# Kernel tuning notes

Hardware: AMD Instinct MI355X
Metric: run time of the kernel (lower is better)

## Reference

```python
import jax, jax.numpy as jnp
import numpy as np

N, D, HF, HS, E, TOPK = 4096, 1024, 2048, 4096, 8, 2
NUM_FRACTAL = 4  # int(8 * 0.5)
EPS_RMS = 1e-6


def setup_inputs() -> dict:
    key = jax.random.key(0)
    ks = jax.random.split(key, 9)
    s = 0.02
    return {
        "x": jax.random.normal(ks[0], (N, D), dtype=jnp.float32),
        "router_w": jax.random.normal(ks[1], (E, D), dtype=jnp.float32) * s,
        "frac_rms": jnp.ones((NUM_FRACTAL, D), jnp.float32),
        "frac_w1": jax.random.normal(ks[2], (NUM_FRACTAL, HF, D), dtype=jnp.float32) * s,
        "frac_w2": jax.random.normal(ks[3], (NUM_FRACTAL, D, HF), dtype=jnp.float32) * s,
        "frac_w3": jax.random.normal(ks[4], (NUM_FRACTAL, HF, D), dtype=jnp.float32) * s,
        "frac_gamma": jnp.full((NUM_FRACTAL, D), 1e-5, jnp.float32),
        "sw_w1": jax.random.normal(ks[5], (E - NUM_FRACTAL, HS, D), dtype=jnp.float32) * s,
        "sw_w2": jax.random.normal(ks[6], (E - NUM_FRACTAL, D, HS), dtype=jnp.float32) * s,
        "sw_w3": jax.random.normal(ks[7], (E - NUM_FRACTAL, HS, D), dtype=jnp.float32) * s,
    }


def _rmsnorm(x, w):
    return x * jax.lax.rsqrt(jnp.mean(x * x, axis=-1, keepdims=True) + EPS_RMS) * w


def _swiglu(x, w1, w2, w3):
    # torch Linear: y = x @ W.T
    return (jax.nn.silu(x @ w1.T) * (x @ w3.T)) @ w2.T


def _fractal(x, rms_w, w1, w2, w3, gamma):
    # depth=1 FractalBlock, eval mode (stochastic depth = identity)
    xn = _rmsnorm(x, rms_w)
    xn = xn + _swiglu(xn, w1, w2, w3)
    return gamma * xn + x


def _moe(x, router_w, frac_rms, frac_w1, frac_w2, frac_w3, frac_gamma,
         sw_w1, sw_w2, sw_w3):
    gate_logits = x @ router_w.T                      # [N, E]
    weights = jax.nn.softmax(gate_logits, axis=-1)
    top_w, top_i = jax.lax.top_k(weights, TOPK)        # [N, K]
    top_w = top_w / jnp.maximum(jnp.sum(top_w, axis=-1, keepdims=True), 1e-9)
    # dense combine weights: zero for unrouted experts (mathematically equal
    # to the gather/index_add dispatch in the original)
    combine = jnp.zeros((x.shape[0], E), x.dtype).at[
        jnp.arange(x.shape[0])[:, None], top_i].add(top_w)  # [N, E]

    out = jnp.zeros_like(x)
    for e in range(NUM_FRACTAL):
        out = out + combine[:, e:e + 1] * _fractal(
            x, frac_rms[e], frac_w1[e], frac_w2[e], frac_w3[e], frac_gamma[e])
    for j in range(E - NUM_FRACTAL):
        e = NUM_FRACTAL + j
        out = out + combine[:, e:e + 1] * _swiglu(x, sw_w1[j], sw_w2[j], sw_w3[j])
    return out


def reference(x, router_w, frac_rms, frac_w1, frac_w2, frac_w3, frac_gamma,
              sw_w1, sw_w2, sw_w3):
    return _moe(x, router_w, frac_rms, frac_w1, frac_w2, frac_w3, frac_gamma,
                sw_w1, sw_w2, sw_w3)
```

## Files before the change

kernel.cpp:

```cpp
#include <hip/hip_runtime.h>
#include <stdint.h>

#define N_TOK 4096
#define DIM   1024
#define HFRAC 2048
#define HSW   4096
#define NEXP  8
#define NFRAC 4
#define TOPK  2
#define TOTAL_ROWS (N_TOK * TOPK)
#define PAD_ROWS   (TOTAL_ROWS + 128)

typedef unsigned short u16;
typedef __bf16 bf16x8 __attribute__((ext_vector_type(8)));
typedef float  floatx4 __attribute__((ext_vector_type(4)));

struct alignas(8)  us4 { u16 v[4]; };
struct alignas(16) us8 { u16 v[8]; };

__device__ __forceinline__ u16 f32_to_bf16_raw(float f) {
    union { float f; uint32_t u; } v; v.f = f;
    uint32_t u = v.u;
    uint32_t r = 0x7FFFu + ((u >> 16) & 1u);
    return (u16)((u + r) >> 16);
}
__device__ __forceinline__ float bf16_raw_to_f32(u16 h) {
    union { uint32_t u; float f; } v; v.u = ((uint32_t)h) << 16;
    return v.f;
}

__device__ __forceinline__ int sw_addr(int row, int chunk) {
    return row * 64 + ((chunk ^ (row & 7)) << 3);
}

__global__ __launch_bounds__(256) void router_kernel(
    const float* __restrict__ x, const float* __restrict__ rw,
    int* __restrict__ re, float* __restrict__ rc, int* __restrict__ counts) {
    const int token = blockIdx.x * 4 + (threadIdx.x >> 6);
    const int lane  = threadIdx.x & 63;
    const float* xr = x + (size_t)token * DIM;

    float acc[NEXP];
#pragma unroll
    for (int e = 0; e < NEXP; ++e) acc[e] = 0.0f;
#pragma unroll
    for (int i = 0; i < DIM / 64; ++i) {
        int k = lane + i * 64;
        float xv = xr[k];
#pragma unroll
        for (int e = 0; e < NEXP; ++e) acc[e] += xv * rw[e * DIM + k];
    }
#pragma unroll
    for (int e = 0; e < NEXP; ++e) {
#pragma unroll
        for (int off = 32; off > 0; off >>= 1) acc[e] += __shfl_down(acc[e], off);
    }
    if (lane == 0) {
        float mx = acc[0];
#pragma unroll
        for (int e = 1; e < NEXP; ++e) mx = fmaxf(mx, acc[e]);
        float w[NEXP]; float s = 0.0f;
#pragma unroll
        for (int e = 0; e < NEXP; ++e) { w[e] = expf(acc[e] - mx); s += w[e]; }
        float inv = 1.0f / s;
#pragma unroll
        for (int e = 0; e < NEXP; ++e) w[e] *= inv;
        int i1 = 0;
#pragma unroll
        for (int e = 1; e < NEXP; ++e) if (w[e] > w[i1]) i1 = e;
        int i2 = (i1 == 0) ? 1 : 0;
#pragma unroll
        for (int e = 0; e < NEXP; ++e) if (e != i1 && w[e] > w[i2]) i2 = e;
        float denom = fmaxf(w[i1] + w[i2], 1e-9f);
        re[token]         = i1; rc[token]         = w[i1] / denom;
        re[N_TOK + token] = i2; rc[N_TOK + token] = w[i2] / denom;
        atomicAdd(&counts[i1], 1);
        atomicAdd(&counts[i2], 1);
    }
}

__global__ void offsets_kernel(const int* __restrict__ counts,
                               int* __restrict__ offs) {
    if (threadIdx.x == 0 && blockIdx.x == 0) {
        int a = 0;
#pragma unroll
        for (int e = 0; e < NEXP; ++e) { offs[e] = a; a += counts[e]; }
    }
}

__global__ __launch_bounds__(256) void scatter_kernel(
    const int* __restrict__ re, const float* __restrict__ rc,
    const int* __restrict__ offs, int* __restrict__ cursor,
    int* __restrict__ rowtok, float* __restrict__ co) {
    int token = blockIdx.x * 256 + threadIdx.x;
#pragma unroll
    for (int slot = 0; slot < TOPK; ++slot) {
        int e = re[slot * N_TOK + token];
        int i = atomicAdd(&cursor[e], 1);
        int r = offs[e] + i;
        rowtok[r] = token | (slot << 16);
        co[r]     = rc[slot * N_TOK + token];
    }
}

__global__ __launch_bounds__(256) void gather_norm_kernel(
    const float* __restrict__ x, const float* __restrict__ frac_rms,
    const int* __restrict__ rowtok, const int* __restrict__ offs,
    u16* __restrict__ Ag) {
    const int r   = blockIdx.x;
    const int tid = threadIdx.x;
    if (r >= TOTAL_ROWS) {
        us4 z = {0, 0, 0, 0};
        reinterpret_cast<us4*>(Ag + (size_t)r * DIM)[tid] = z;
        return;
    }
    int e = 0;
#pragma unroll
    for (int i = 1; i < NEXP; ++i) if (r >= offs[i]) e = i;
    const int token = rowtok[r] & 0xFFFF;
    float4 v = reinterpret_cast<const float4*>(x + (size_t)token * DIM)[tid];
    if (e < NFRAC) {
        float ss = v.x * v.x + v.y * v.y + v.z * v.z + v.w * v.w;
#pragma unroll
        for (int off = 32; off > 0; off >>= 1) ss += __shfl_down(ss, off);
        __shared__ float red[4];
        if ((tid & 63) == 0) red[tid >> 6] = ss;
        __syncthreads();
        float scale = rsqrtf((red[0] + red[1] + red[2] + red[3]) * (1.0f / DIM) + 1e-6f);
        float4 wv = reinterpret_cast<const float4*>(frac_rms + (size_t)e * DIM)[tid];
        v.x *= scale * wv.x; v.y *= scale * wv.y;
        v.z *= scale * wv.z; v.w *= scale * wv.w;
    }
    us4 o = { f32_to_bf16_raw(v.x), f32_to_bf16_raw(v.y),
              f32_to_bf16_raw(v.z), f32_to_bf16_raw(v.w) };
    reinterpret_cast<us4*>(Ag + (size_t)r * DIM)[tid] = o;
}

#define BM 128
#define BN 64
#define BK 64

__global__ __launch_bounds__(256) void gemm1_kernel(
    const u16* __restrict__ Ag,
    const float* __restrict__ frac_w1, const float* __restrict__ frac_w3,
    const float* __restrict__ sw_w1,   const float* __restrict__ sw_w3,
    u16* __restrict__ gbuf,
    const int* __restrict__ counts, const int* __restrict__ offs) {
    const int e   = blockIdx.z;
    const int cnt = counts[e];
    const int m0  = blockIdx.y * BM;
    if (m0 >= cnt) return;
    const int Ne = (e < NFRAC) ? HFRAC : HSW;
    const int n0 = blockIdx.x * BN;
    if (n0 >= Ne) return;
    const int rowbase = offs[e];
    const float* W1 = (e < NFRAC) ? frac_w1 + (size_t)e * HFRAC * DIM
                                  : sw_w1 + (size_t)(e - NFRAC) * HSW * DIM;
    const float* W3 = (e < NFRAC) ? frac_w3 + (size_t)e * HFRAC * DIM
                                  : sw_w3 + (size_t)(e - NFRAC) * HSW * DIM;
    const u16* A = Ag + (size_t)(rowbase + m0) * DIM;

    __shared__ u16 sA[BM * BK];
    __shared__ u16 sB1[BN * BK];
    __shared__ u16 sB3[BN * BK];

    const int tid  = threadIdx.x;
    const int wave = tid >> 6;
    const int lane = tid & 63;

    floatx4 acc1[2][4], acc3[2][4];
    floatx4 zero = { 0.f, 0.f, 0.f, 0.f };
#pragma unroll
    for (int mt = 0; mt < 2; ++mt)
#pragma unroll
        for (int nt = 0; nt < 4; ++nt) { acc1[mt][nt] = zero; acc3[mt][nt] = zero; }

    for (int k0 = 0; k0 < DIM; k0 += BK) {
#pragma unroll
        for (int it = 0; it < 4; ++it) {
            int idx = it * 2048 + tid * 8;
            int r = idx >> 6, c = idx & 63;
            int4 v = *reinterpret_cast<const int4*>(A + (size_t)r * DIM + k0 + c);
            *reinterpret_cast<int4*>(&sA[sw_addr(r, c >> 3)]) = v;
        }
#pragma unroll
        for (int it = 0; it < 2; ++it) {
            int idx = it * 2048 + tid * 8;
            int r = idx >> 6, c = idx & 63;
            size_t go = (size_t)(n0 + r) * DIM + k0 + c;
            float4 a1 = *reinterpret_cast<const float4*>(W1 + go);
            float4 b1 = *reinterpret_cast<const float4*>(W1 + go + 4);
            float4 a3 = *reinterpret_cast<const float4*>(W3 + go);
            float4 b3 = *reinterpret_cast<const float4*>(W3 + go + 4);
            us8 o1 = { f32_to_bf16_raw(a1.x), f32_to_bf16_raw(a1.y),
                       f32_to_bf16_raw(a1.z), f32_to_bf16_raw(a1.w),
                       f32_to_bf16_raw(b1.x), f32_to_bf16_raw(b1.y),
                       f32_to_bf16_raw(b1.z), f32_to_bf16_raw(b1.w) };
            us8 o3 = { f32_to_bf16_raw(a3.x), f32_to_bf16_raw(a3.y),
                       f32_to_bf16_raw(a3.z), f32_to_bf16_raw(a3.w),
                       f32_to_bf16_raw(b3.x), f32_to_bf16_raw(b3.y),
                       f32_to_bf16_raw(b3.z), f32_to_bf16_raw(b3.w) };
            *reinterpret_cast<us8*>(&sB1[sw_addr(r, c >> 3)]) = o1;
            *reinterpret_cast<us8*>(&sB3[sw_addr(r, c >> 3)]) = o3;
        }
        __syncthreads();
#pragma unroll
        for (int ks = 0; ks < 2; ++ks) {
            const int chunk = ks * 4 + (lane >> 4);
            bf16x8 af[2], b1f[4], b3f[4];
#pragma unroll
            for (int mt = 0; mt < 2; ++mt) {
                int ra = wave * 32 + mt * 16 + (lane & 15);
                af[mt] = *reinterpret_cast<const bf16x8*>(&sA[sw_addr(ra, chunk)]);
            }
#pragma unroll
            for (int nt = 0; nt < 4; ++nt) {
                int rb = nt * 16 + (lane & 15);
                b1f[nt] = *reinterpret_cast<const bf16x8*>(&sB1[sw_addr(rb, chunk)]);
                b3f[nt] = *reinterpret_cast<const bf16x8*>(&sB3[sw_addr(rb, chunk)]);
            }
#pragma unroll
            for (int mt = 0; mt < 2; ++mt)
#pragma unroll
                for (int nt = 0; nt < 4; ++nt) {
                    acc1[mt][nt] = __builtin_amdgcn_mfma_f32_16x16x32_bf16(
                        af[mt], b1f[nt], acc1[mt][nt], 0, 0, 0);
                    acc3[mt][nt] = __builtin_amdgcn_mfma_f32_16x16x32_bf16(
                        af[mt], b3f[nt], acc3[mt][nt], 0, 0, 0);
                }
        }
        __syncthreads();
    }
#pragma unroll
    for (int mt = 0; mt < 2; ++mt)
#pragma unroll
        for (int nt = 0; nt < 4; ++nt)
#pragma unroll
            for (int r = 0; r < 4; ++r) {
                int row_local = m0 + wave * 32 + mt * 16 + (lane >> 4) * 4 + r;
                if (row_local >= cnt) continue;
                int col = n0 + nt * 16 + (lane & 15);
                float h1 = acc1[mt][nt][r];
                float h3 = acc3[mt][nt][r];
                float g = (h1 / (1.0f + expf(-h1))) * h3;
                gbuf[(size_t)(rowbase + row_local) * HSW + col] = f32_to_bf16_raw(g);
            }
}

__global__ __launch_bounds__(256) void gemm2_kernel(
    const u16* __restrict__ gbuf,
    const float* __restrict__ frac_w2, const float* __restrict__ sw_w2,
    const u16* __restrict__ Ag, const float* __restrict__ x,
    const float* __restrict__ frac_gamma,
    const int* __restrict__ rowtok, const float* __restrict__ co,
    const int* __restrict__ counts, const int* __restrict__ offs,
    float* __restrict__ ybuf) {
    const int e   = blockIdx.z;
    const int cnt = counts[e];
    const int m0  = blockIdx.y * BM;
    if (m0 >= cnt) return;
    const int n0 = blockIdx.x * BN;
    const int Ke = (e < NFRAC) ? HFRAC : HSW;
    const int rowbase = offs[e];
    const float* W2 = (e < NFRAC) ? frac_w2 + (size_t)e * DIM * HFRAC
                                  : sw_w2 + (size_t)(e - NFRAC) * DIM * HSW;
    const u16* A = gbuf + (size_t)(rowbase + m0) * HSW;

    __shared__ u16 sA[BM * BK];
    __shared__ u16 sB[BN * BK];

    const int tid  = threadIdx.x;
    const int wave = tid >> 6;
    const int lane = tid & 63;

    floatx4 acc[2][4];
    floatx4 zero = { 0.f, 0.f, 0.f, 0.f };
#pragma unroll
    for (int mt = 0; mt < 2; ++mt)
#pragma unroll
        for (int nt = 0; nt < 4; ++nt) acc[mt][nt] = zero;

    for (int k0 = 0; k0 < Ke; k0 += BK) {
#pragma unroll
        for (int it = 0; it < 4; ++it) {
            int idx = it * 2048 + tid * 8;
            int r = idx >> 6, c = idx & 63;
            int4 v = *reinterpret_cast<const int4*>(A + (size_t)r * HSW + k0 + c);
            *reinterpret_cast<int4*>(&sA[sw_addr(r, c >> 3)]) = v;
        }
#pragma unroll
        for (int it = 0; it < 2; ++it) {
            int idx = it * 2048 + tid * 8;
            int r = idx >> 6, c = idx & 63;
            size_t go = (size_t)(n0 + r) * Ke + k0 + c;
            float4 a = *reinterpret_cast<const float4*>(W2 + go);
            float4 b = *reinterpret_cast<const float4*>(W2 + go + 4);
            us8 o = { f32_to_bf16_raw(a.x), f32_to_bf16_raw(a.y),
                      f32_to_bf16_raw(a.z), f32_to_bf16_raw(a.w),
                      f32_to_bf16_raw(b.x), f32_to_bf16_raw(b.y),
                      f32_to_bf16_raw(b.z), f32_to_bf16_raw(b.w) };
            *reinterpret_cast<us8*>(&sB[sw_addr(r, c >> 3)]) = o;
        }
        __syncthreads();
#pragma unroll
        for (int ks = 0; ks < 2; ++ks) {
            const int chunk = ks * 4 + (lane >> 4);
            bf16x8 af[2], bf[4];
#pragma unroll
            for (int mt = 0; mt < 2; ++mt) {
                int ra = wave * 32 + mt * 16 + (lane & 15);
                af[mt] = *reinterpret_cast<const bf16x8*>(&sA[sw_addr(ra, chunk)]);
            }
#pragma unroll
            for (int nt = 0; nt < 4; ++nt) {
                int rb = nt * 16 + (lane & 15);
                bf[nt] = *reinterpret_cast<const bf16x8*>(&sB[sw_addr(rb, chunk)]);
            }
#pragma unroll
            for (int mt = 0; mt < 2; ++mt)
#pragma unroll
                for (int nt = 0; nt < 4; ++nt)
                    acc[mt][nt] = __builtin_amdgcn_mfma_f32_16x16x32_bf16(
                        af[mt], bf[nt], acc[mt][nt], 0, 0, 0);
        }
        __syncthreads();
    }
    const float* gamma = frac_gamma + (size_t)e * DIM;
#pragma unroll
    for (int mt = 0; mt < 2; ++mt)
#pragma unroll
        for (int nt = 0; nt < 4; ++nt)
#pragma unroll
            for (int rr = 0; rr < 4; ++rr) {
                int row_local = m0 + wave * 32 + mt * 16 + (lane >> 4) * 4 + rr;
                if (row_local >= cnt) continue;
                int r = rowbase + row_local;
                int col = n0 + nt * 16 + (lane & 15);
                int info  = rowtok[r];
                int token = info & 0xFFFF;
                int slot  = info >> 16;
                float coef = co[r];
                float y = acc[mt][nt][rr];
                float val;
                if (e < NFRAC) {
                    float xn = bf16_raw_to_f32(Ag[(size_t)r * DIM + col]);
                    val = coef * (gamma[col] * (xn + y) + x[(size_t)token * DIM + col]);
                } else {
                    val = coef * y;
                }
                ybuf[(size_t)slot * N_TOK * DIM + (size_t)token * DIM + col] = val;
            }
}

__global__ __launch_bounds__(256) void combine_kernel(
    const float* __restrict__ ybuf, float* __restrict__ out) {
    size_t i = (size_t)blockIdx.x * 256 + threadIdx.x;
    float4 a = reinterpret_cast<const float4*>(ybuf)[i];
    float4 b = reinterpret_cast<const float4*>(ybuf + (size_t)N_TOK * DIM)[i];
    float4 o = { a.x + b.x, a.y + b.y, a.z + b.z, a.w + b.w };
    reinterpret_cast<float4*>(out)[i] = o;
}

extern "C" void kernel_launch(void* const* d_in, const int* in_sizes, int n_in,
                              void* d_out, int out_size, void* d_ws, size_t ws_size,
                              hipStream_t stream) {
    const float* x          = (const float*)d_in[0];
    const float* router_w   = (const float*)d_in[1];
    const float* frac_rms   = (const float*)d_in[2];
    const float* frac_w1    = (const float*)d_in[3];
    const float* frac_w2    = (const float*)d_in[4];
    const float* frac_w3    = (const float*)d_in[5];
    const float* frac_gamma = (const float*)d_in[6];
    const float* sw_w1      = (const float*)d_in[7];
    const float* sw_w2      = (const float*)d_in[8];
    const float* sw_w3      = (const float*)d_in[9];
    float* out = (float*)d_out;

    char* ws = (char*)d_ws;
    int*   counts = (int*)ws;
    int*   cursor = (int*)(ws + 32);
    int*   offs   = (int*)(ws + 64);
    int*   re     = (int*)(ws + 256);
    float* rc     = (float*)(ws + 256 + (32u << 10));
    int*   rowtok = (int*)(ws + 256 + (64u << 10));
    float* co     = (float*)(ws + 256 + (112u << 10));
    u16*   Ag     = (u16*)(ws + (1u << 18));
    u16*   gbuf   = (u16*)(ws + (size_t)18 * (1u << 20));
    float* ybuf   = (float*)(ws + (size_t)88 * (1u << 20));

    hipMemsetAsync(ws, 0, 256, stream);

    router_kernel<<<N_TOK / 4, 256, 0, stream>>>(x, router_w, re, rc, counts);
    offsets_kernel<<<1, 64, 0, stream>>>(counts, offs);
    scatter_kernel<<<N_TOK / 256, 256, 0, stream>>>(re, rc, offs, cursor, rowtok, co);
    gather_norm_kernel<<<PAD_ROWS, 256, 0, stream>>>(x, frac_rms, rowtok, offs, Ag);

    gemm1_kernel<<<dim3(HSW / BN, TOTAL_ROWS / BM, NEXP), 256, 0, stream>>>(
        Ag, frac_w1, frac_w3, sw_w1, sw_w3, gbuf, counts, offs);

    gemm2_kernel<<<dim3(DIM / BN, TOTAL_ROWS / BM, NEXP), 256, 0, stream>>>(
        gbuf, frac_w2, sw_w2, Ag, x, frac_gamma, rowtok, co, counts, offs, ybuf);

    combine_kernel<<<(N_TOK * DIM) / (4 * 256), 256, 0, stream>>>(ybuf, out);
}
```

Before: 834.1 us.

## Pre-convert weights to bf16, stage tiles via async LDS loads, atomic combine

Each expert weight matrix is converted to bf16 once per call in separate conversion kernels, instead of being converted from fp32 repeatedly inside every GEMM tile. The GEMMs now stage swizzled tiles straight from global memory into LDS with global_load_lds, and the N tile grows to 128 with a 2x2 wave layout that doubles accumulators per wave. The ybuf staging buffer and the combine kernel are dropped, and gemm2 atomically adds into a zeroed output instead. In exchange this adds weight-conversion passes plus workspace reuse, more register pressure, and non-deterministic fp32 atomic accumulation.

```diff
diff --git a/kernel.cpp b/kernel.cpp
--- a/kernel.cpp
+++ b/kernel.cpp
@@ -16,7 +16,6 @@
 typedef float  floatx4 __attribute__((ext_vector_type(4)));
 
 struct alignas(8)  us4 { u16 v[4]; };
-struct alignas(16) us8 { u16 v[8]; };
 
 __device__ __forceinline__ u16 f32_to_bf16_raw(float f) {
     union { float f; uint32_t u; } v; v.f = f;
@@ -29,8 +28,33 @@
     return v.f;
 }
 
-__device__ __forceinline__ int sw_addr(int row, int chunk) {
-    return row * 64 + ((chunk ^ (row & 7)) << 3);
+__device__ __forceinline__ void async_copy16(const u16* g, u16* s) {
+    __builtin_amdgcn_global_load_lds(
+        (const __attribute__((address_space(1))) uint32_t*)g,
+        (__attribute__((address_space(3))) uint32_t*)s, 16, 0, 0);
+}
+
+__device__ __forceinline__ void stage_tile(const u16* g, int ld, u16* s,
+                                           int wave, int lane) {
+    const int r0 = wave * 32 + (lane >> 3);
+    const int c8 = ((lane & 7) ^ ((lane >> 3) & 7)) << 3;
+    const u16* gp = g + (size_t)r0 * ld + c8;
+#pragma unroll
+    for (int it = 0; it < 4; ++it)
+        async_copy16(gp + (size_t)(it * 8) * ld, s + (wave * 32 + it * 8) * 64);
+}
+
+__device__ __forceinline__ bf16x8 frag_ld(const u16* s, int row, int q) {
+    return *reinterpret_cast<const bf16x8*>(&s[row * 64 + ((q ^ (row & 7)) << 3)]);
+}
+
+__global__ __launch_bounds__(256) void cvt_kernel(
+    const float* __restrict__ in, u16* __restrict__ out) {
+    size_t i = (size_t)blockIdx.x * 256 + threadIdx.x;
+    float4 v = reinterpret_cast<const float4*>(in)[i];
+    us4 o = { f32_to_bf16_raw(v.x), f32_to_bf16_raw(v.y),
+              f32_to_bf16_raw(v.z), f32_to_bf16_raw(v.w) };
+    reinterpret_cast<us4*>(out)[i] = o;
 }
 
 __global__ __launch_bounds__(256) void router_kernel(
@@ -137,13 +161,13 @@
 }
 
 #define BM 128
-#define BN 64
+#define BN 128
 #define BK 64
 
 __global__ __launch_bounds__(256) void gemm1_kernel(
     const u16* __restrict__ Ag,
-    const float* __restrict__ frac_w1, const float* __restrict__ frac_w3,
-    const float* __restrict__ sw_w1,   const float* __restrict__ sw_w3,
+    const u16* __restrict__ w1f, const u16* __restrict__ w3f,
+    const u16* __restrict__ w1s, const u16* __restrict__ w3s,
     u16* __restrict__ gbuf,
     const int* __restrict__ counts, const int* __restrict__ offs) {
     const int e   = blockIdx.z;
@@ -154,10 +178,10 @@
     const int n0 = blockIdx.x * BN;
     if (n0 >= Ne) return;
     const int rowbase = offs[e];
-    const float* W1 = (e < NFRAC) ? frac_w1 + (size_t)e * HFRAC * DIM
-                                  : sw_w1 + (size_t)(e - NFRAC) * HSW * DIM;
-    const float* W3 = (e < NFRAC) ? frac_w3 + (size_t)e * HFRAC * DIM
-                                  : sw_w3 + (size_t)(e - NFRAC) * HSW * DIM;
+    const u16* W1 = (e < NFRAC) ? w1f + (size_t)e * HFRAC * DIM
+                                : w1s + (size_t)(e - NFRAC) * HSW * DIM;
+    const u16* W3 = (e < NFRAC) ? w3f + (size_t)e * HFRAC * DIM
+                                : w3s + (size_t)(e - NFRAC) * HSW * DIM;
     const u16* A = Ag + (size_t)(rowbase + m0) * DIM;
 
     __shared__ u16 sA[BM * BK];
@@ -167,79 +191,56 @@
     const int tid  = threadIdx.x;
     const int wave = tid >> 6;
     const int lane = tid & 63;
-
-    floatx4 acc1[2][4], acc3[2][4];
+    const int wm = wave >> 1, wn = wave & 1;
+    const int fr = lane & 15;
+    const int quad = lane >> 4;
+
+    floatx4 acc1[4][4], acc3[4][4];
     floatx4 zero = { 0.f, 0.f, 0.f, 0.f };
 #pragma unroll
-    for (int mt = 0; mt < 2; ++mt)
+    for (int mt = 0; mt < 4; ++mt)
 #pragma unroll
         for (int nt = 0; nt < 4; ++nt) { acc1[mt][nt] = zero; acc3[mt][nt] = zero; }
 
+    const u16* gB1 = W1 + (size_t)n0 * DIM;
+    const u16* gB3 = W3 + (size_t)n0 * DIM;
+
     for (int k0 = 0; k0 < DIM; k0 += BK) {
-#pragma unroll
-        for (int it = 0; it < 4; ++it) {
-            int idx = it * 2048 + tid * 8;
-            int r = idx >> 6, c = idx & 63;
-            int4 v = *reinterpret_cast<const int4*>(A + (size_t)r * DIM + k0 + c);
-            *reinterpret_cast<int4*>(&sA[sw_addr(r, c >> 3)]) = v;
+        stage_tile(A   + k0, DIM, sA,  wave, lane);
+        stage_tile(gB1 + k0, DIM, sB1, wave, lane);
+        stage_tile(gB3 + k0, DIM, sB3, wave, lane);
+        __syncthreads();
+#pragma unroll
+        for (int ks = 0; ks < 2; ++ks) {
+            const int q = ks * 4 + quad;
+            bf16x8 af[4];
+#pragma unroll
+            for (int mt = 0; mt < 4; ++mt)
+                af[mt] = frag_ld(sA, wm * 64 + mt * 16 + fr, q);
+#pragma unroll
+            for (int nt = 0; nt < 4; ++nt) {
+                bf16x8 b1 = frag_ld(sB1, wn * 64 + nt * 16 + fr, q);
+                bf16x8 b3 = frag_ld(sB3, wn * 64 + nt * 16 + fr, q);
+#pragma unroll
+                for (int mt = 0; mt < 4; ++mt) {
+                    acc1[mt][nt] = __builtin_amdgcn_mfma_f32_16x16x32_bf16(
+                        af[mt], b1, acc1[mt][nt], 0, 0, 0);
+                    acc3[mt][nt] = __builtin_amdgcn_mfma_f32_16x16x32_bf16(
+                        af[mt], b3, acc3[mt][nt], 0, 0, 0);
+                }
+            }
         }
-#pragma unroll
-        for (int it = 0; it < 2; ++it) {
-            int idx = it * 2048 + tid * 8;
-            int r = idx >> 6, c = idx & 63;
-            size_t go = (size_t)(n0 + r) * DIM + k0 + c;
-            float4 a1 = *reinterpret_cast<const float4*>(W1 + go);
-            float4 b1 = *reinterpret_cast<const float4*>(W1 + go + 4);
-            float4 a3 = *reinterpret_cast<const float4*>(W3 + go);
-            float4 b3 = *reinterpret_cast<const float4*>(W3 + go + 4);
-            us8 o1 = { f32_to_bf16_raw(a1.x), f32_to_bf16_raw(a1.y),
-                       f32_to_bf16_raw(a1.z), f32_to_bf16_raw(a1.w),
-                       f32_to_bf16_raw(b1.x), f32_to_bf16_raw(b1.y),
-                       f32_to_bf16_raw(b1.z), f32_to_bf16_raw(b1.w) };
-            us8 o3 = { f32_to_bf16_raw(a3.x), f32_to_bf16_raw(a3.y),
-                       f32_to_bf16_raw(a3.z), f32_to_bf16_raw(a3.w),
-                       f32_to_bf16_raw(b3.x), f32_to_bf16_raw(b3.y),
-                       f32_to_bf16_raw(b3.z), f32_to_bf16_raw(b3.w) };
-            *reinterpret_cast<us8*>(&sB1[sw_addr(r, c >> 3)]) = o1;
-            *reinterpret_cast<us8*>(&sB3[sw_addr(r, c >> 3)]) = o3;
-        }
-        __syncthreads();
-#pragma unroll
-        for (int ks = 0; ks < 2; ++ks) {
-            const int chunk = ks * 4 + (lane >> 4);
-            bf16x8 af[2], b1f[4], b3f[4];
-#pragma unroll
-            for (int mt = 0; mt < 2; ++mt) {
-                int ra = wave * 32 + mt * 16 + (lane & 15);
-                af[mt] = *reinterpret_cast<const bf16x8*>(&sA[sw_addr(ra, chunk)]);
-            }
-#pragma unroll
-            for (int nt = 0; nt < 4; ++nt) {
-                int rb = nt * 16 + (lane & 15);
-                b1f[nt] = *reinterpret_cast<const bf16x8*>(&sB1[sw_addr(rb, chunk)]);
-                b3f[nt] = *reinterpret_cast<const bf16x8*>(&sB3[sw_addr(rb, chunk)]);
-            }
-#pragma unroll
-            for (int mt = 0; mt < 2; ++mt)
-#pragma unroll
-                for (int nt = 0; nt < 4; ++nt) {
-                    acc1[mt][nt] = __builtin_amdgcn_mfma_f32_16x16x32_bf16(
-                        af[mt], b1f[nt], acc1[mt][nt], 0, 0, 0);
-                    acc3[mt][nt] = __builtin_amdgcn_mfma_f32_16x16x32_bf16(
-                        af[mt], b3f[nt], acc3[mt][nt], 0, 0, 0);
-                }
-        }
-        __syncthreads();
-    }
-#pragma unroll
-    for (int mt = 0; mt < 2; ++mt)
+        __syncthreads();
+    }
+#pragma unroll
+    for (int mt = 0; mt < 4; ++mt)
 #pragma unroll
         for (int nt = 0; nt < 4; ++nt)
 #pragma unroll
             for (int r = 0; r < 4; ++r) {
-                int row_local = m0 + wave * 32 + mt * 16 + (lane >> 4) * 4 + r;
+                int row_local = m0 + wm * 64 + mt * 16 + quad * 4 + r;
                 if (row_local >= cnt) continue;
-                int col = n0 + nt * 16 + (lane & 15);
+                int col = n0 + wn * 64 + nt * 16 + fr;
                 float h1 = acc1[mt][nt][r];
                 float h3 = acc3[mt][nt][r];
                 float g = (h1 / (1.0f + expf(-h1))) * h3;
@@ -249,12 +250,12 @@
 
 __global__ __launch_bounds__(256) void gemm2_kernel(
     const u16* __restrict__ gbuf,
-    const float* __restrict__ frac_w2, const float* __restrict__ sw_w2,
+    const u16* __restrict__ w2f, const u16* __restrict__ w2s,
     const u16* __restrict__ Ag, const float* __restrict__ x,
     const float* __restrict__ frac_gamma,
     const int* __restrict__ rowtok, const float* __restrict__ co,
     const int* __restrict__ counts, const int* __restrict__ offs,
-    float* __restrict__ ybuf) {
+    float* __restrict__ out) {
     const int e   = blockIdx.z;
     const int cnt = counts[e];
     const int m0  = blockIdx.y * BM;
@@ -262,8 +263,8 @@
     const int n0 = blockIdx.x * BN;
     const int Ke = (e < NFRAC) ? HFRAC : HSW;
     const int rowbase = offs[e];
-    const float* W2 = (e < NFRAC) ? frac_w2 + (size_t)e * DIM * HFRAC
-                                  : sw_w2 + (size_t)(e - NFRAC) * DIM * HSW;
+    const u16* W2 = (e < NFRAC) ? w2f + (size_t)e * DIM * HFRAC
+                                : w2s + (size_t)(e - NFRAC) * DIM * HSW;
     const u16* A = gbuf + (size_t)(rowbase + m0) * HSW;
 
     __shared__ u16 sA[BM * BK];
@@ -272,73 +273,54 @@
     const int tid  = threadIdx.x;
     const int wave = tid >> 6;
     const int lane = tid & 63;
-
-    floatx4 acc[2][4];
+    const int wm = wave >> 1, wn = wave & 1;
+    const int fr = lane & 15;
+    const int quad = lane >> 4;
+
+    floatx4 acc[4][4];
     floatx4 zero = { 0.f, 0.f, 0.f, 0.f };
 #pragma unroll
-    for (int mt = 0; mt < 2; ++mt)
+    for (int mt = 0; mt < 4; ++mt)
 #pragma unroll
         for (int nt = 0; nt < 4; ++nt) acc[mt][nt] = zero;
 
+    const u16* gB = W2 + (size_t)n0 * Ke;
+
     for (int k0 = 0; k0 < Ke; k0 += BK) {
-#pragma unroll
-        for (int it = 0; it < 4; ++it) {
-            int idx = it * 2048 + tid * 8;
-            int r = idx >> 6, c = idx & 63;
-            int4 v = *reinterpret_cast<const int4*>(A + (size_t)r * HSW + k0 + c);
-            *reinterpret_cast<int4*>(&sA[sw_addr(r, c >> 3)]) = v;
+        stage_tile(A  + k0, HSW, sA, wave, lane);
+        stage_tile(gB + k0, Ke,  sB, wave, lane);
+        __syncthreads();
+#pragma unroll
+        for (int ks = 0; ks < 2; ++ks) {
+            const int q = ks * 4 + quad;
+            bf16x8 af[4];
+#pragma unroll
+            for (int mt = 0; mt < 4; ++mt)
+                af[mt] = frag_ld(sA, wm * 64 + mt * 16 + fr, q);
+#pragma unroll
+            for (int nt = 0; nt < 4; ++nt) {
+                bf16x8 b = frag_ld(sB, wn * 64 + nt * 16 + fr, q);
+#pragma unroll
+                for (int mt = 0; mt < 4; ++mt)
+                    acc[mt][nt] = __builtin_amdgcn_mfma_f32_16x16x32_bf16(
+                        af[mt], b, acc[mt][nt], 0, 0, 0);
+            }
         }
-#pragma unroll
-        for (int it = 0; it < 2; ++it) {
-            int idx = it * 2048 + tid * 8;
-            int r = idx >> 6, c = idx & 63;
-            size_t go = (size_t)(n0 + r) * Ke + k0 + c;
-            float4 a = *reinterpret_cast<const float4*>(W2 + go);
-            float4 b = *reinterpret_cast<const float4*>(W2 + go + 4);
-            us8 o = { f32_to_bf16_raw(a.x), f32_to_bf16_raw(a.y),
-                      f32_to_bf16_raw(a.z), f32_to_bf16_raw(a.w),
-                      f32_to_bf16_raw(b.x), f32_to_bf16_raw(b.y),
-                      f32_to_bf16_raw(b.z), f32_to_bf16_raw(b.w) };
-            *reinterpret_cast<us8*>(&sB[sw_addr(r, c >> 3)]) = o;
-        }
-        __syncthreads();
-#pragma unroll
-        for (int ks = 0; ks < 2; ++ks) {
-            const int chunk = ks * 4 + (lane >> 4);
-            bf16x8 af[2], bf[4];
-#pragma unroll
-            for (int mt = 0; mt < 2; ++mt) {
-                int ra = wave * 32 + mt * 16 + (lane & 15);
-                af[mt] = *reinterpret_cast<const bf16x8*>(&sA[sw_addr(ra, chunk)]);
-            }
-#pragma unroll
-            for (int nt = 0; nt < 4; ++nt) {
-                int rb = nt * 16 + (lane & 15);
-                bf[nt] = *reinterpret_cast<const bf16x8*>(&sB[sw_addr(rb, chunk)]);
-            }
-#pragma unroll
-            for (int mt = 0; mt < 2; ++mt)
-#pragma unroll
-                for (int nt = 0; nt < 4; ++nt)
-                    acc[mt][nt] = __builtin_amdgcn_mfma_f32_16x16x32_bf16(
-                        af[mt], bf[nt], acc[mt][nt], 0, 0, 0);
-        }
         __syncthreads();
     }
     const float* gamma = frac_gamma + (size_t)e * DIM;
 #pragma unroll
-    for (int mt = 0; mt < 2; ++mt)
+    for (int mt = 0; mt < 4; ++mt)
 #pragma unroll
         for (int nt = 0; nt < 4; ++nt)
 #pragma unroll
             for (int rr = 0; rr < 4; ++rr) {
-                int row_local = m0 + wave * 32 + mt * 16 + (lane >> 4) * 4 + rr;
+                int row_local = m0 + wm * 64 + mt * 16 + quad * 4 + rr;
                 if (row_local >= cnt) continue;
                 int r = rowbase + row_local;
-                int col = n0 + nt * 16 + (lane & 15);
+                int col = n0 + wn * 64 + nt * 16 + fr;
                 int info  = rowtok[r];
                 int token = info & 0xFFFF;
-                int slot  = info >> 16;
                 float coef = co[r];
                 float y = acc[mt][nt][rr];
                 float val;
@@ -348,17 +330,8 @@
                 } else {
                     val = coef * y;
                 }
-                ybuf[(size_t)slot * N_TOK * DIM + (size_t)token * DIM + col] = val;
+                atomicAdd(&out[(size_t)token * DIM + col], val);
             }
-}
-
-__global__ __launch_bounds__(256) void combine_kernel(
-    const float* __restrict__ ybuf, float* __restrict__ out) {
-    size_t i = (size_t)blockIdx.x * 256 + threadIdx.x;
-    float4 a = reinterpret_cast<const float4*>(ybuf)[i];
-    float4 b = reinterpret_cast<const float4*>(ybuf + (size_t)N_TOK * DIM)[i];
-    float4 o = { a.x + b.x, a.y + b.y, a.z + b.z, a.w + b.w };
-    reinterpret_cast<float4*>(out)[i] = o;
 }
 
 extern "C" void kernel_launch(void* const* d_in, const int* in_sizes, int n_in,
@@ -376,19 +349,31 @@
     const float* sw_w3      = (const float*)d_in[9];
     float* out = (float*)d_out;
 
+    const size_t MB = 1u << 20;
     char* ws = (char*)d_ws;
     int*   counts = (int*)ws;
     int*   cursor = (int*)(ws + 32);
     int*   offs   = (int*)(ws + 64);
-    int*   re     = (int*)(ws + 256);
-    float* rc     = (float*)(ws + 256 + (32u << 10));
-    int*   rowtok = (int*)(ws + 256 + (64u << 10));
-    float* co     = (float*)(ws + 256 + (112u << 10));
-    u16*   Ag     = (u16*)(ws + (1u << 18));
-    u16*   gbuf   = (u16*)(ws + (size_t)18 * (1u << 20));
-    float* ybuf   = (float*)(ws + (size_t)88 * (1u << 20));
+    int*   re     = (int*)(ws + 1024);
+    float* rc     = (float*)(ws + 36864);
+    int*   rowtok = (int*)(ws + 73728);
+    float* co     = (float*)(ws + 110592);
+    u16* Ag   = (u16*)(ws + 1 * MB);
+    u16* gbuf = (u16*)(ws + 19 * MB);
+    u16* w1f  = (u16*)(ws + 84 * MB);
+    u16* w3f  = (u16*)(ws + 100 * MB);
+    u16* w1s  = (u16*)(ws + 116 * MB);
+    u16* w3s  = (u16*)(ws + 148 * MB);
+    u16* w2f  = (u16*)(ws + 84 * MB);
+    u16* w2s  = (u16*)(ws + 100 * MB);
 
     hipMemsetAsync(ws, 0, 256, stream);
+    hipMemsetAsync(d_out, 0, (size_t)N_TOK * DIM * sizeof(float), stream);
+
+    cvt_kernel<<<(NFRAC * HFRAC * DIM) / 1024, 256, 0, stream>>>(frac_w1, w1f);
+    cvt_kernel<<<(NFRAC * HFRAC * DIM) / 1024, 256, 0, stream>>>(frac_w3, w3f);
+    cvt_kernel<<<(NFRAC * HSW * DIM) / 1024, 256, 0, stream>>>(sw_w1, w1s);
+    cvt_kernel<<<(NFRAC * HSW * DIM) / 1024, 256, 0, stream>>>(sw_w3, w3s);
 
     router_kernel<<<N_TOK / 4, 256, 0, stream>>>(x, router_w, re, rc, counts);
     offsets_kernel<<<1, 64, 0, stream>>>(counts, offs);
@@ -396,10 +381,11 @@
     gather_norm_kernel<<<PAD_ROWS, 256, 0, stream>>>(x, frac_rms, rowtok, offs, Ag);
 
     gemm1_kernel<<<dim3(HSW / BN, TOTAL_ROWS / BM, NEXP), 256, 0, stream>>>(
-        Ag, frac_w1, frac_w3, sw_w1, sw_w3, gbuf, counts, offs);
+        Ag, w1f, w3f, w1s, w3s, gbuf, counts, offs);
+
+    cvt_kernel<<<(NFRAC * DIM * HFRAC) / 1024, 256, 0, stream>>>(frac_w2, w2f);
+    cvt_kernel<<<(NFRAC * DIM * HSW) / 1024, 256, 0, stream>>>(sw_w2, w2s);
 
     gemm2_kernel<<<dim3(DIM / BN, TOTAL_ROWS / BM, NEXP), 256, 0, stream>>>(
-        gbuf, frac_w2, sw_w2, Ag, x, frac_gamma, rowtok, co, counts, offs, ybuf);
-
-    combine_kernel<<<(N_TOK * DIM) / (4 * 256), 256, 0, stream>>>(ybuf, out);
-}
+        gbuf, w2f, w2s, Ag, x, frac_gamma, rowtok, co, counts, offs, out);
+}
```

New measurement: 977.1 us. +17.1%, slower.
